# Kernel optimization log

Measured on AMD Instinct MI355X. Metric: run time of the kernel, lower is better.

Reference implementation:

```python
import jax, jax.numpy as jnp
import numpy as np


def setup_inputs() -> dict:
    key = jax.random.key(0)
    B, C, T = 64, 256, 2048
    X = jax.random.normal(key, (B, C, T), dtype=jnp.float32)
    return {"X": X}


def reference(X) -> jnp.ndarray:
    # torch.cov(correction=0) per sample: rows = variables, cols = observations
    T = X.shape[-1]
    Xc = X - jnp.mean(X, axis=-1, keepdims=True)      # [B, C, T]
    cov = jnp.einsum('bct,bdt->bcd', Xc, Xc) / T       # [B, C, C]
    return cov
```

## Files before the change

kernel.cpp:

```cpp
#include <hip/hip_runtime.h>


#define NB 64
#define NC 256
#define NT 2048
#define NITER 32

typedef __bf16 bf16x8 __attribute__((ext_vector_type(8)));
typedef float  f32x8  __attribute__((ext_vector_type(8)));
typedef float  f32x4  __attribute__((ext_vector_type(4)));

__global__ __launch_bounds__(512, 2) void cov_kernel(const float* __restrict__ X,
                                                     float* __restrict__ out) {
    __shared__ __align__(16) unsigned char smem[68608];
    __bf16* sAB  = (__bf16*)smem;
    float*  redF = (float*)smem;

    const int bid  = blockIdx.x;
    const int xcd  = bid & 7;
    const int g    = bid >> 3;
    const int b    = xcd + 8 * (g >> 2);
    const int q    = g & 3;
    const int row0 = (q >> 1) * 128, col0 = (q & 1) * 128;

    const float* __restrict__ Xb = X + (size_t)b * (NC * NT);

    const int t    = threadIdx.x;
    const int lane = t & 63;
    const int wave = t >> 6;
    const int h    = wave >> 2;
    const int wq   = wave & 3;
    const int wm   = wq >> 1, wn = wq & 1;
    const int quad = lane >> 4;
    const int l16  = lane & 15;

    const int u  = t & 255;
    const int sr = u >> 2;
    const int sc = (u & 3) * 8;
    const float* gA0 = Xb + (size_t)(row0 + sr) * NT + h * (NT / 2) + sc;
    const float* gA1 = gA0 + (size_t)64 * NT;
    const float* gB0 = Xb + (size_t)(col0 + sr) * NT + h * (NT / 2) + sc;
    const float* gB1 = gB0 + (size_t)64 * NT;

    __bf16* sA[2] = { sAB + (0 * 2 + h) * 4096, sAB + (1 * 2 + h) * 4096 };
    __bf16* sB[2] = { sAB + 16384 + (0 * 2 + h) * 4096, sAB + 16384 + (1 * 2 + h) * 4096 };
    const int woff = sr * 32 + sc;

    f32x4 acc[4][4], accRS[4], accCS[4];
#pragma unroll
    for (int i = 0; i < 4; ++i) {
        accRS[i] = (f32x4){0.f, 0.f, 0.f, 0.f};
        accCS[i] = (f32x4){0.f, 0.f, 0.f, 0.f};
#pragma unroll
        for (int j = 0; j < 4; ++j) acc[i][j] = (f32x4){0.f, 0.f, 0.f, 0.f};
    }
    const bf16x8 ones = {(__bf16)1.0f, (__bf16)1.0f, (__bf16)1.0f, (__bf16)1.0f,
                         (__bf16)1.0f, (__bf16)1.0f, (__bf16)1.0f, (__bf16)1.0f};

    f32x8 pA0 = *(const f32x8*)gA0;
    f32x8 pA1 = *(const f32x8*)gA1;
    f32x8 pB0 = *(const f32x8*)gB0;
    f32x8 pB1 = *(const f32x8*)gB1;
    *(bf16x8*)(sA[0] + woff)        = __builtin_convertvector(pA0, bf16x8);
    *(bf16x8*)(sA[0] + woff + 2048) = __builtin_convertvector(pA1, bf16x8);
    *(bf16x8*)(sB[0] + woff)        = __builtin_convertvector(pB0, bf16x8);
    *(bf16x8*)(sB[0] + woff + 2048) = __builtin_convertvector(pB1, bf16x8);
    pA0 = *(const f32x8*)(gA0 + 32);
    pA1 = *(const f32x8*)(gA1 + 32);
    pB0 = *(const f32x8*)(gB0 + 32);
    pB1 = *(const f32x8*)(gB1 + 32);
    __syncthreads();

    const int aBase = (wm * 64 + l16) * 32 + quad * 8;
    const int bBase = (wn * 64 + l16) * 32 + quad * 8;

#pragma unroll 2
    for (int k = 0; k < NITER; ++k) {
        const int cur = k & 1, nxt = cur ^ 1;

        if (k + 1 < NITER) {
            *(bf16x8*)(sA[nxt] + woff)        = __builtin_convertvector(pA0, bf16x8);
            *(bf16x8*)(sA[nxt] + woff + 2048) = __builtin_convertvector(pA1, bf16x8);
            *(bf16x8*)(sB[nxt] + woff)        = __builtin_convertvector(pB0, bf16x8);
            *(bf16x8*)(sB[nxt] + woff + 2048) = __builtin_convertvector(pB1, bf16x8);
        }
        if (k + 2 < NITER) {
            pA0 = *(const f32x8*)(gA0 + (k + 2) * 32);
            pA1 = *(const f32x8*)(gA1 + (k + 2) * 32);
            pB0 = *(const f32x8*)(gB0 + (k + 2) * 32);
            pB1 = *(const f32x8*)(gB1 + (k + 2) * 32);
        }

        bf16x8 aF[4], bF[4];
#pragma unroll
        for (int mt = 0; mt < 4; ++mt)
            aF[mt] = *(const bf16x8*)(sA[cur] + aBase + mt * 16 * 32);
#pragma unroll
        for (int nt = 0; nt < 4; ++nt)
            bF[nt] = *(const bf16x8*)(sB[cur] + bBase + nt * 16 * 32);

#pragma unroll
        for (int mt = 0; mt < 4; ++mt) {
            accRS[mt] = __builtin_amdgcn_mfma_f32_16x16x32_bf16(aF[mt], ones, accRS[mt], 0, 0, 0);
#pragma unroll
            for (int nt = 0; nt < 4; ++nt)
                acc[mt][nt] = __builtin_amdgcn_mfma_f32_16x16x32_bf16(aF[mt], bF[nt], acc[mt][nt], 0, 0, 0);
        }
#pragma unroll
        for (int nt = 0; nt < 4; ++nt)
            accCS[nt] = __builtin_amdgcn_mfma_f32_16x16x32_bf16(ones, bF[nt], accCS[nt], 0, 0, 0);

        __syncthreads();
    }

    float* red = redF + wq * (64 * 65);
    float* rs  = redF + 4 * (64 * 65);
    float* cs  = rs + 256;

    if (h == 1) {
#pragma unroll
        for (int mt = 0; mt < 4; ++mt)
#pragma unroll
            for (int nt = 0; nt < 4; ++nt)
#pragma unroll
                for (int r = 0; r < 4; ++r)
                    red[(mt * 16 + quad * 4 + r) * 65 + nt * 16 + l16] = acc[mt][nt][r];
        if (l16 == 0) {
#pragma unroll
            for (int mt = 0; mt < 4; ++mt)
#pragma unroll
                for (int r = 0; r < 4; ++r)
                    rs[wq * 64 + mt * 16 + quad * 4 + r] = accRS[mt][r];
        }
        if (quad == 0) {
#pragma unroll
            for (int nt = 0; nt < 4; ++nt)
                cs[wq * 64 + nt * 16 + l16] = accCS[nt][0];
        }
    }
    __syncthreads();

    if (h == 0) {
        const float invT = 1.0f / NT;
        float* __restrict__ outB = out + (size_t)b * (NC * NC);
#pragma unroll
        for (int mt = 0; mt < 4; ++mt) {
#pragma unroll
            for (int nt = 0; nt < 4; ++nt) {
#pragma unroll
                for (int r = 0; r < 4; ++r) {
                    const int R = mt * 16 + quad * 4 + r;
                    const int C = nt * 16 + l16;
                    const float tot = red[R * 65 + C] + acc[mt][nt][r];
                    const float Sx  = rs[wq * 64 + R] + accRS[mt][r];
                    const float Sy  = cs[wq * 64 + C] + accCS[nt][0];
                    outB[(size_t)(row0 + wm * 64 + R) * NC + (col0 + wn * 64 + C)] =
                        (tot - Sx * Sy * invT) * invT;
                }
            }
        }
    }
}

extern "C" void kernel_launch(void* const* d_in, const int* in_sizes, int n_in,
                              void* d_out, int out_size, void* d_ws, size_t ws_size,
                              hipStream_t stream) {
    const float* X = (const float*)d_in[0];
    float* out = (float*)d_out;
    (void)in_sizes; (void)n_in; (void)out_size; (void)d_ws; (void)ws_size;
    cov_kernel<<<256, 512, 0, stream>>>(X, out);
}
```

Baseline: 207.4 us.

## Split Gram computation over T chunks with full 256x256 tiles and separate reduce kernel

```diff
diff --git a/kernel.cpp b/kernel.cpp
--- a/kernel.cpp
+++ b/kernel.cpp
@@ -4,162 +4,147 @@
 #define NB 64
 #define NC 256
 #define NT 2048
-#define NITER 32
+#define NKC 4
+#define KC (NT / NKC)
+#define BK 32
+#define NIT (KC / BK)
+
+#define G_STRIDE ((size_t)NB * NC * NC)
+#define SX_OFF   ((size_t)NKC * G_STRIDE)
+#define SX_STRIDE (NB * NC)
 
 typedef __bf16 bf16x8 __attribute__((ext_vector_type(8)));
 typedef float  f32x8  __attribute__((ext_vector_type(8)));
 typedef float  f32x4  __attribute__((ext_vector_type(4)));
 
-__global__ __launch_bounds__(512, 2) void cov_kernel(const float* __restrict__ X,
-                                                     float* __restrict__ out) {
-    __shared__ __align__(16) unsigned char smem[68608];
-    __bf16* sAB  = (__bf16*)smem;
-    float*  redF = (float*)smem;
+__global__ __launch_bounds__(512, 2) void cov_gram(const float* __restrict__ X,
+                                                   float* __restrict__ ws) {
+    __shared__ __align__(16) __bf16 sX[2][NC * BK];
 
-    const int bid  = blockIdx.x;
-    const int xcd  = bid & 7;
-    const int g    = bid >> 3;
-    const int b    = xcd + 8 * (g >> 2);
-    const int q    = g & 3;
-    const int row0 = (q >> 1) * 128, col0 = (q & 1) * 128;
-
-    const float* __restrict__ Xb = X + (size_t)b * (NC * NT);
+    const int bid = blockIdx.x;
+    const int b   = bid >> 2;
+    const int kc  = bid & 3;
+    const float* __restrict__ Xb = X + (size_t)b * (NC * NT) + kc * KC;
 
     const int t    = threadIdx.x;
     const int lane = t & 63;
     const int wave = t >> 6;
-    const int h    = wave >> 2;
-    const int wq   = wave & 3;
-    const int wm   = wq >> 1, wn = wq & 1;
+    const int wm   = wave >> 2;
+    const int wn   = wave & 3;
     const int quad = lane >> 4;
     const int l16  = lane & 15;
 
-    const int u  = t & 255;
-    const int sr = u >> 2;
-    const int sc = (u & 3) * 8;
-    const float* gA0 = Xb + (size_t)(row0 + sr) * NT + h * (NT / 2) + sc;
-    const float* gA1 = gA0 + (size_t)64 * NT;
-    const float* gB0 = Xb + (size_t)(col0 + sr) * NT + h * (NT / 2) + sc;
-    const float* gB1 = gB0 + (size_t)64 * NT;
+    const int sr = t >> 1;
+    const int sc = (t & 1) * 16;
+    const float* g0 = Xb + (size_t)sr * NT + sc;
+    const int woff = sr * BK + sc;
 
-    __bf16* sA[2] = { sAB + (0 * 2 + h) * 4096, sAB + (1 * 2 + h) * 4096 };
-    __bf16* sB[2] = { sAB + 16384 + (0 * 2 + h) * 4096, sAB + 16384 + (1 * 2 + h) * 4096 };
-    const int woff = sr * 32 + sc;
+    f32x4 acc[8][4], accRS[2];
+#pragma unroll
+    for (int mt = 0; mt < 8; ++mt)
+#pragma unroll
+        for (int nt = 0; nt < 4; ++nt)
+            acc[mt][nt] = (f32x4){0.f, 0.f, 0.f, 0.f};
+    accRS[0] = (f32x4){0.f, 0.f, 0.f, 0.f};
+    accRS[1] = (f32x4){0.f, 0.f, 0.f, 0.f};
 
-    f32x4 acc[4][4], accRS[4], accCS[4];
-#pragma unroll
-    for (int i = 0; i < 4; ++i) {
-        accRS[i] = (f32x4){0.f, 0.f, 0.f, 0.f};
-        accCS[i] = (f32x4){0.f, 0.f, 0.f, 0.f};
-#pragma unroll
-        for (int j = 0; j < 4; ++j) acc[i][j] = (f32x4){0.f, 0.f, 0.f, 0.f};
-    }
     const bf16x8 ones = {(__bf16)1.0f, (__bf16)1.0f, (__bf16)1.0f, (__bf16)1.0f,
                          (__bf16)1.0f, (__bf16)1.0f, (__bf16)1.0f, (__bf16)1.0f};
 
-    f32x8 pA0 = *(const f32x8*)gA0;
-    f32x8 pA1 = *(const f32x8*)gA1;
-    f32x8 pB0 = *(const f32x8*)gB0;
-    f32x8 pB1 = *(const f32x8*)gB1;
-    *(bf16x8*)(sA[0] + woff)        = __builtin_convertvector(pA0, bf16x8);
-    *(bf16x8*)(sA[0] + woff + 2048) = __builtin_convertvector(pA1, bf16x8);
-    *(bf16x8*)(sB[0] + woff)        = __builtin_convertvector(pB0, bf16x8);
-    *(bf16x8*)(sB[0] + woff + 2048) = __builtin_convertvector(pB1, bf16x8);
-    pA0 = *(const f32x8*)(gA0 + 32);
-    pA1 = *(const f32x8*)(gA1 + 32);
-    pB0 = *(const f32x8*)(gB0 + 32);
-    pB1 = *(const f32x8*)(gB1 + 32);
+    f32x8 p0 = *(const f32x8*)g0;
+    f32x8 p1 = *(const f32x8*)(g0 + 8);
+    *(bf16x8*)&sX[0][woff]     = __builtin_convertvector(p0, bf16x8);
+    *(bf16x8*)&sX[0][woff + 8] = __builtin_convertvector(p1, bf16x8);
+    p0 = *(const f32x8*)(g0 + BK);
+    p1 = *(const f32x8*)(g0 + BK + 8);
     __syncthreads();
 
-    const int aBase = (wm * 64 + l16) * 32 + quad * 8;
-    const int bBase = (wn * 64 + l16) * 32 + quad * 8;
+    const int aBase  = (wm * 128 + l16) * BK + quad * 8;
+    const int bBase  = (wn * 64 + l16) * BK + quad * 8;
+    const int rsBase = (wm * 128 + wn * 32 + l16) * BK + quad * 8;
 
 #pragma unroll 2
-    for (int k = 0; k < NITER; ++k) {
+    for (int k = 0; k < NIT; ++k) {
         const int cur = k & 1, nxt = cur ^ 1;
 
-        if (k + 1 < NITER) {
-            *(bf16x8*)(sA[nxt] + woff)        = __builtin_convertvector(pA0, bf16x8);
-            *(bf16x8*)(sA[nxt] + woff + 2048) = __builtin_convertvector(pA1, bf16x8);
-            *(bf16x8*)(sB[nxt] + woff)        = __builtin_convertvector(pB0, bf16x8);
-            *(bf16x8*)(sB[nxt] + woff + 2048) = __builtin_convertvector(pB1, bf16x8);
+        if (k + 1 < NIT) {
+            *(bf16x8*)&sX[nxt][woff]     = __builtin_convertvector(p0, bf16x8);
+            *(bf16x8*)&sX[nxt][woff + 8] = __builtin_convertvector(p1, bf16x8);
         }
-        if (k + 2 < NITER) {
-            pA0 = *(const f32x8*)(gA0 + (k + 2) * 32);
-            pA1 = *(const f32x8*)(gA1 + (k + 2) * 32);
-            pB0 = *(const f32x8*)(gB0 + (k + 2) * 32);
-            pB1 = *(const f32x8*)(gB1 + (k + 2) * 32);
+        if (k + 2 < NIT) {
+            p0 = *(const f32x8*)(g0 + (k + 2) * BK);
+            p1 = *(const f32x8*)(g0 + (k + 2) * BK + 8);
         }
 
-        bf16x8 aF[4], bF[4];
+        bf16x8 aF[8], bF[4];
 #pragma unroll
-        for (int mt = 0; mt < 4; ++mt)
-            aF[mt] = *(const bf16x8*)(sA[cur] + aBase + mt * 16 * 32);
+        for (int mt = 0; mt < 8; ++mt)
+            aF[mt] = *(const bf16x8*)&sX[cur][aBase + mt * 16 * BK];
 #pragma unroll
         for (int nt = 0; nt < 4; ++nt)
-            bF[nt] = *(const bf16x8*)(sB[cur] + bBase + nt * 16 * 32);
+            bF[nt] = *(const bf16x8*)&sX[cur][bBase + nt * 16 * BK];
+        bf16x8 rF0 = *(const bf16x8*)&sX[cur][rsBase];
+        bf16x8 rF1 = *(const bf16x8*)&sX[cur][rsBase + 16 * BK];
 
 #pragma unroll
-        for (int mt = 0; mt < 4; ++mt) {
-            accRS[mt] = __builtin_amdgcn_mfma_f32_16x16x32_bf16(aF[mt], ones, accRS[mt], 0, 0, 0);
+        for (int mt = 0; mt < 8; ++mt)
 #pragma unroll
             for (int nt = 0; nt < 4; ++nt)
-                acc[mt][nt] = __builtin_amdgcn_mfma_f32_16x16x32_bf16(aF[mt], bF[nt], acc[mt][nt], 0, 0, 0);
-        }
-#pragma unroll
-        for (int nt = 0; nt < 4; ++nt)
-            accCS[nt] = __builtin_amdgcn_mfma_f32_16x16x32_bf16(ones, bF[nt], accCS[nt], 0, 0, 0);
+                acc[mt][nt] = __builtin_amdgcn_mfma_f32_16x16x32_bf16(
+                    aF[mt], bF[nt], acc[mt][nt], 0, 0, 0);
+        accRS[0] = __builtin_amdgcn_mfma_f32_16x16x32_bf16(rF0, ones, accRS[0], 0, 0, 0);
+        accRS[1] = __builtin_amdgcn_mfma_f32_16x16x32_bf16(rF1, ones, accRS[1], 0, 0, 0);
 
         __syncthreads();
     }
 
-    float* red = redF + wq * (64 * 65);
-    float* rs  = redF + 4 * (64 * 65);
-    float* cs  = rs + 256;
-
-    if (h == 1) {
+    float* __restrict__ Gp = ws + (size_t)kc * G_STRIDE + (size_t)b * (NC * NC);
 #pragma unroll
-        for (int mt = 0; mt < 4; ++mt)
+    for (int mt = 0; mt < 8; ++mt) {
+        const int i0 = wm * 128 + mt * 16 + quad * 4;
 #pragma unroll
-            for (int nt = 0; nt < 4; ++nt)
+        for (int nt = 0; nt < 4; ++nt) {
+            const int j = wn * 64 + nt * 16 + l16;
 #pragma unroll
-                for (int r = 0; r < 4; ++r)
-                    red[(mt * 16 + quad * 4 + r) * 65 + nt * 16 + l16] = acc[mt][nt][r];
-        if (l16 == 0) {
-#pragma unroll
-            for (int mt = 0; mt < 4; ++mt)
-#pragma unroll
-                for (int r = 0; r < 4; ++r)
-                    rs[wq * 64 + mt * 16 + quad * 4 + r] = accRS[mt][r];
-        }
-        if (quad == 0) {
-#pragma unroll
-            for (int nt = 0; nt < 4; ++nt)
-                cs[wq * 64 + nt * 16 + l16] = accCS[nt][0];
+            for (int r = 0; r < 4; ++r)
+                Gp[(size_t)(i0 + r) * NC + j] = acc[mt][nt][r];
         }
     }
-    __syncthreads();
+    if (l16 == 0) {
+        float* __restrict__ Sp = ws + SX_OFF + (size_t)kc * SX_STRIDE + b * NC;
+#pragma unroll
+        for (int s = 0; s < 2; ++s)
+#pragma unroll
+            for (int r = 0; r < 4; ++r)
+                Sp[wm * 128 + wn * 32 + s * 16 + quad * 4 + r] = accRS[s][r];
+    }
+}
 
-    if (h == 0) {
-        const float invT = 1.0f / NT;
-        float* __restrict__ outB = out + (size_t)b * (NC * NC);
-#pragma unroll
-        for (int mt = 0; mt < 4; ++mt) {
-#pragma unroll
-            for (int nt = 0; nt < 4; ++nt) {
-#pragma unroll
-                for (int r = 0; r < 4; ++r) {
-                    const int R = mt * 16 + quad * 4 + r;
-                    const int C = nt * 16 + l16;
-                    const float tot = red[R * 65 + C] + acc[mt][nt][r];
-                    const float Sx  = rs[wq * 64 + R] + accRS[mt][r];
-                    const float Sy  = cs[wq * 64 + C] + accCS[nt][0];
-                    outB[(size_t)(row0 + wm * 64 + R) * NC + (col0 + wn * 64 + C)] =
-                        (tot - Sx * Sy * invT) * invT;
-                }
-            }
-        }
-    }
+__global__ __launch_bounds__(256) void cov_reduce(const float* __restrict__ ws,
+                                                  float* __restrict__ out) {
+    const unsigned e  = blockIdx.x * 256u + threadIdx.x;
+    const int j4 = e & 63;
+    const int i  = (e >> 6) & 255;
+    const int b  = e >> 14;
+    const size_t g = ((size_t)b * NC + i) * NC + j4 * 4;
+
+    f32x4 s = *(const f32x4*)&ws[g];
+    s += *(const f32x4*)&ws[G_STRIDE + g];
+    s += *(const f32x4*)&ws[2 * G_STRIDE + g];
+    s += *(const f32x4*)&ws[3 * G_STRIDE + g];
+
+    const float* __restrict__ Sx = ws + SX_OFF;
+    const int sb = b * NC;
+    float sxi = Sx[sb + i] + Sx[SX_STRIDE + sb + i] +
+                Sx[2 * SX_STRIDE + sb + i] + Sx[3 * SX_STRIDE + sb + i];
+    f32x4 sy = *(const f32x4*)&Sx[sb + j4 * 4];
+    sy += *(const f32x4*)&Sx[SX_STRIDE + sb + j4 * 4];
+    sy += *(const f32x4*)&Sx[2 * SX_STRIDE + sb + j4 * 4];
+    sy += *(const f32x4*)&Sx[3 * SX_STRIDE + sb + j4 * 4];
+
+    const float invT = 1.0f / NT;
+    f32x4 r = (s - sy * (sxi * invT)) * invT;
+    *(f32x4*)&out[g] = r;
 }
 
 extern "C" void kernel_launch(void* const* d_in, const int* in_sizes, int n_in,
@@ -167,6 +152,8 @@
                               hipStream_t stream) {
     const float* X = (const float*)d_in[0];
     float* out = (float*)d_out;
-    (void)in_sizes; (void)n_in; (void)out_size; (void)d_ws; (void)ws_size;
-    cov_kernel<<<256, 512, 0, stream>>>(X, out);
+    float* ws = (float*)d_ws;
+    (void)in_sizes; (void)n_in; (void)out_size; (void)ws_size;
+    cov_gram<<<256, 512, 0, stream>>>(X, ws);
+    cov_reduce<<<4096, 256, 0, stream>>>(ws, out);
 }
```

After: 221.4 us. +6.7%, slower.

## Exploit covariance symmetry: compute three quadrants per batch and mirror off-diagonal

Applied to the files above, without the earlier changes.

```diff
diff --git a/kernel.cpp b/kernel.cpp
--- a/kernel.cpp
+++ b/kernel.cpp
@@ -19,9 +19,11 @@
     const int bid  = blockIdx.x;
     const int xcd  = bid & 7;
     const int g    = bid >> 3;
-    const int b    = xcd + 8 * (g >> 2);
-    const int q    = g & 3;
-    const int row0 = (q >> 1) * 128, col0 = (q & 1) * 128;
+    const int b    = xcd + 8 * (g / 3);
+    const int qi   = g % 3;
+    const int row0 = (qi == 1) ? 128 : 0;
+    const int col0 = (qi == 0) ? 0 : 128;
+    const bool diag = (qi != 2);
 
     const float* __restrict__ Xb = X + (size_t)b * (NC * NT);
 
@@ -43,7 +45,12 @@
     const float* gB1 = gB0 + (size_t)64 * NT;
 
     __bf16* sA[2] = { sAB + (0 * 2 + h) * 4096, sAB + (1 * 2 + h) * 4096 };
-    __bf16* sB[2] = { sAB + 16384 + (0 * 2 + h) * 4096, sAB + 16384 + (1 * 2 + h) * 4096 };
+    __bf16* sB[2];
+    if (diag) { sB[0] = sA[0]; sB[1] = sA[1]; }
+    else {
+        sB[0] = sAB + 16384 + (0 * 2 + h) * 4096;
+        sB[1] = sAB + 16384 + (1 * 2 + h) * 4096;
+    }
     const int woff = sr * 32 + sc;
 
     f32x4 acc[4][4], accRS[4], accCS[4];
@@ -59,16 +66,20 @@
 
     f32x8 pA0 = *(const f32x8*)gA0;
     f32x8 pA1 = *(const f32x8*)gA1;
-    f32x8 pB0 = *(const f32x8*)gB0;
-    f32x8 pB1 = *(const f32x8*)gB1;
+    f32x8 pB0 = pA0, pB1 = pA1;
+    if (!diag) { pB0 = *(const f32x8*)gB0; pB1 = *(const f32x8*)gB1; }
     *(bf16x8*)(sA[0] + woff)        = __builtin_convertvector(pA0, bf16x8);
     *(bf16x8*)(sA[0] + woff + 2048) = __builtin_convertvector(pA1, bf16x8);
-    *(bf16x8*)(sB[0] + woff)        = __builtin_convertvector(pB0, bf16x8);
-    *(bf16x8*)(sB[0] + woff + 2048) = __builtin_convertvector(pB1, bf16x8);
+    if (!diag) {
+        *(bf16x8*)(sB[0] + woff)        = __builtin_convertvector(pB0, bf16x8);
+        *(bf16x8*)(sB[0] + woff + 2048) = __builtin_convertvector(pB1, bf16x8);
+    }
     pA0 = *(const f32x8*)(gA0 + 32);
     pA1 = *(const f32x8*)(gA1 + 32);
-    pB0 = *(const f32x8*)(gB0 + 32);
-    pB1 = *(const f32x8*)(gB1 + 32);
+    if (!diag) {
+        pB0 = *(const f32x8*)(gB0 + 32);
+        pB1 = *(const f32x8*)(gB1 + 32);
+    }
     __syncthreads();
 
     const int aBase = (wm * 64 + l16) * 32 + quad * 8;
@@ -81,14 +92,18 @@
         if (k + 1 < NITER) {
             *(bf16x8*)(sA[nxt] + woff)        = __builtin_convertvector(pA0, bf16x8);
             *(bf16x8*)(sA[nxt] + woff + 2048) = __builtin_convertvector(pA1, bf16x8);
-            *(bf16x8*)(sB[nxt] + woff)        = __builtin_convertvector(pB0, bf16x8);
-            *(bf16x8*)(sB[nxt] + woff + 2048) = __builtin_convertvector(pB1, bf16x8);
+            if (!diag) {
+                *(bf16x8*)(sB[nxt] + woff)        = __builtin_convertvector(pB0, bf16x8);
+                *(bf16x8*)(sB[nxt] + woff + 2048) = __builtin_convertvector(pB1, bf16x8);
+            }
         }
         if (k + 2 < NITER) {
             pA0 = *(const f32x8*)(gA0 + (k + 2) * 32);
             pA1 = *(const f32x8*)(gA1 + (k + 2) * 32);
-            pB0 = *(const f32x8*)(gB0 + (k + 2) * 32);
-            pB1 = *(const f32x8*)(gB1 + (k + 2) * 32);
+            if (!diag) {
+                pB0 = *(const f32x8*)(gB0 + (k + 2) * 32);
+                pB1 = *(const f32x8*)(gB1 + (k + 2) * 32);
+            }
         }
 
         bf16x8 aF[4], bF[4];
@@ -140,9 +155,10 @@
     }
     __syncthreads();
 
+    const float invT = 1.0f / NT;
+    float* __restrict__ outB = out + (size_t)b * (NC * NC);
+
     if (h == 0) {
-        const float invT = 1.0f / NT;
-        float* __restrict__ outB = out + (size_t)b * (NC * NC);
 #pragma unroll
         for (int mt = 0; mt < 4; ++mt) {
 #pragma unroll
@@ -154,8 +170,27 @@
                     const float tot = red[R * 65 + C] + acc[mt][nt][r];
                     const float Sx  = rs[wq * 64 + R] + accRS[mt][r];
                     const float Sy  = cs[wq * 64 + C] + accCS[nt][0];
-                    outB[(size_t)(row0 + wm * 64 + R) * NC + (col0 + wn * 64 + C)] =
-                        (tot - Sx * Sy * invT) * invT;
+                    const float val = (tot - Sx * Sy * invT) * invT;
+                    outB[(size_t)(row0 + wm * 64 + R) * NC + (col0 + wn * 64 + C)] = val;
+                    if (qi == 2) red[R * 65 + C] = val;
+                }
+            }
+        }
+    }
+
+    if (qi == 2) {
+        __syncthreads();
+        if (h == 1) {
+#pragma unroll
+            for (int mt = 0; mt < 4; ++mt) {
+                const int jj = mt * 16 + quad * 4;
+#pragma unroll
+                for (int nt = 0; nt < 4; ++nt) {
+                    const int ii = nt * 16 + l16;
+#pragma unroll
+                    for (int r = 0; r < 4; ++r)
+                        outB[(size_t)(col0 + wn * 64 + jj + r) * NC +
+                             (row0 + wm * 64 + ii)] = red[ii * 65 + jj + r];
                 }
             }
         }
@@ -168,5 +203,5 @@
     const float* X = (const float*)d_in[0];
     float* out = (float*)d_out;
     (void)in_sizes; (void)n_in; (void)out_size; (void)d_ws; (void)ws_size;
-    cov_kernel<<<256, 512, 0, stream>>>(X, out);
+    cov_kernel<<<192, 512, 0, stream>>>(X, out);
 }
```

After: 207.6 us. No clear change (+0.1%).

## Load MFMA fragments directly from global memory, drop LDS staging and barriers

Applied to the files above, without the earlier changes.

```diff
diff --git a/kernel.cpp b/kernel.cpp
--- a/kernel.cpp
+++ b/kernel.cpp
@@ -12,9 +12,7 @@
 
 __global__ __launch_bounds__(512, 2) void cov_kernel(const float* __restrict__ X,
                                                      float* __restrict__ out) {
-    __shared__ __align__(16) unsigned char smem[68608];
-    __bf16* sAB  = (__bf16*)smem;
-    float*  redF = (float*)smem;
+    __shared__ __align__(16) float redF[4 * 64 * 65 + 512];
 
     const int bid  = blockIdx.x;
     const int xcd  = bid & 7;
@@ -34,17 +32,14 @@
     const int quad = lane >> 4;
     const int l16  = lane & 15;
 
-    const int u  = t & 255;
-    const int sr = u >> 2;
-    const int sc = (u & 3) * 8;
-    const float* gA0 = Xb + (size_t)(row0 + sr) * NT + h * (NT / 2) + sc;
-    const float* gA1 = gA0 + (size_t)64 * NT;
-    const float* gB0 = Xb + (size_t)(col0 + sr) * NT + h * (NT / 2) + sc;
-    const float* gB1 = gB0 + (size_t)64 * NT;
-
-    __bf16* sA[2] = { sAB + (0 * 2 + h) * 4096, sAB + (1 * 2 + h) * 4096 };
-    __bf16* sB[2] = { sAB + 16384 + (0 * 2 + h) * 4096, sAB + 16384 + (1 * 2 + h) * 4096 };
-    const int woff = sr * 32 + sc;
+    const float* aP[4];
+    const float* bP[4];
+#pragma unroll
+    for (int mt = 0; mt < 4; ++mt)
+        aP[mt] = Xb + (size_t)(row0 + wm * 64 + mt * 16 + l16) * NT + h * (NT / 2) + quad * 8;
+#pragma unroll
+    for (int nt = 0; nt < 4; ++nt)
+        bP[nt] = Xb + (size_t)(col0 + wn * 64 + nt * 16 + l16) * NT + h * (NT / 2) + quad * 8;
 
     f32x4 acc[4][4], accRS[4], accCS[4];
 #pragma unroll
@@ -57,48 +52,21 @@
     const bf16x8 ones = {(__bf16)1.0f, (__bf16)1.0f, (__bf16)1.0f, (__bf16)1.0f,
                          (__bf16)1.0f, (__bf16)1.0f, (__bf16)1.0f, (__bf16)1.0f};
 
-    f32x8 pA0 = *(const f32x8*)gA0;
-    f32x8 pA1 = *(const f32x8*)gA1;
-    f32x8 pB0 = *(const f32x8*)gB0;
-    f32x8 pB1 = *(const f32x8*)gB1;
-    *(bf16x8*)(sA[0] + woff)        = __builtin_convertvector(pA0, bf16x8);
-    *(bf16x8*)(sA[0] + woff + 2048) = __builtin_convertvector(pA1, bf16x8);
-    *(bf16x8*)(sB[0] + woff)        = __builtin_convertvector(pB0, bf16x8);
-    *(bf16x8*)(sB[0] + woff + 2048) = __builtin_convertvector(pB1, bf16x8);
-    pA0 = *(const f32x8*)(gA0 + 32);
-    pA1 = *(const f32x8*)(gA1 + 32);
-    pB0 = *(const f32x8*)(gB0 + 32);
-    pB1 = *(const f32x8*)(gB1 + 32);
-    __syncthreads();
-
-    const int aBase = (wm * 64 + l16) * 32 + quad * 8;
-    const int bBase = (wn * 64 + l16) * 32 + quad * 8;
-
 #pragma unroll 2
     for (int k = 0; k < NITER; ++k) {
-        const int cur = k & 1, nxt = cur ^ 1;
-
-        if (k + 1 < NITER) {
-            *(bf16x8*)(sA[nxt] + woff)        = __builtin_convertvector(pA0, bf16x8);
-            *(bf16x8*)(sA[nxt] + woff + 2048) = __builtin_convertvector(pA1, bf16x8);
-            *(bf16x8*)(sB[nxt] + woff)        = __builtin_convertvector(pB0, bf16x8);
-            *(bf16x8*)(sB[nxt] + woff + 2048) = __builtin_convertvector(pB1, bf16x8);
-        }
-        if (k + 2 < NITER) {
-            pA0 = *(const f32x8*)(gA0 + (k + 2) * 32);
-            pA1 = *(const f32x8*)(gA1 + (k + 2) * 32);
-            pB0 = *(const f32x8*)(gB0 + (k + 2) * 32);
-            pB1 = *(const f32x8*)(gB1 + (k + 2) * 32);
-        }
+        f32x8 a32[4], b32[4];
+#pragma unroll
+        for (int mt = 0; mt < 4; ++mt) a32[mt] = *(const f32x8*)(aP[mt] + k * 32);
+#pragma unroll
+        for (int nt = 0; nt < 4; ++nt) b32[nt] = *(const f32x8*)(bP[nt] + k * 32);
 
         bf16x8 aF[4], bF[4];
 #pragma unroll
-        for (int mt = 0; mt < 4; ++mt)
-            aF[mt] = *(const bf16x8*)(sA[cur] + aBase + mt * 16 * 32);
+        for (int mt = 0; mt < 4; ++mt) aF[mt] = __builtin_convertvector(a32[mt], bf16x8);
 #pragma unroll
-        for (int nt = 0; nt < 4; ++nt)
-            bF[nt] = *(const bf16x8*)(sB[cur] + bBase + nt * 16 * 32);
+        for (int nt = 0; nt < 4; ++nt) bF[nt] = __builtin_convertvector(b32[nt], bf16x8);
 
+        __builtin_amdgcn_s_setprio(1);
 #pragma unroll
         for (int mt = 0; mt < 4; ++mt) {
             accRS[mt] = __builtin_amdgcn_mfma_f32_16x16x32_bf16(aF[mt], ones, accRS[mt], 0, 0, 0);
@@ -109,8 +77,7 @@
 #pragma unroll
         for (int nt = 0; nt < 4; ++nt)
             accCS[nt] = __builtin_amdgcn_mfma_f32_16x16x32_bf16(ones, bF[nt], accCS[nt], 0, 0, 0);
-
-        __syncthreads();
+        __builtin_amdgcn_s_setprio(0);
     }
 
     float* red = redF + wq * (64 * 65);
```

Measured after the change: 270.1 us. +30.3%, slower.
